# Kernel tuning notes

Hardware: AMD Instinct MI355X
Metric: run time of the kernel (lower is better)

The kernel has to match this reference:

```python
import jax, jax.numpy as jnp
import numpy as np

RADII = (4, 8, 16)
BETA = 0.3
TEMP = 0.07
EPS = 1e-6


def box_filter(x, r):
    """Windowed sum over a (2r+1)x(2r+1) window with zero padding (same as
    F.conv2d with a ones kernel and padding=r), applied to the last two axes.
    Uses cumulative sums (integral image) instead of an explicit convolution."""
    def along(x, axis):
        n = x.shape[axis]
        c = jnp.cumsum(x, axis=axis)
        pad = [(0, 0)] * x.ndim
        pad[axis] = (1, 0)
        c = jnp.pad(c, pad)  # prepend a zero so c[i] = sum of first i elems
        i = jnp.arange(n)
        hi = jnp.clip(i + r + 1, 0, n)
        lo = jnp.clip(i - r, 0, n)
        return jnp.take(c, hi, axis=axis) - jnp.take(c, lo, axis=axis)
    return along(along(x, -2), -1)


def build_prototypes(support_feats, mask_f, anchor_pos, anchor_sample, anchor_radius):
    """mask_f: [S,H,W] float. Returns (local_protos [M,C], local_weights [M], global_proto [C])."""
    fg = mask_f.sum()
    global_proto = (support_feats * mask_f[:, None]).sum((0, 2, 3)) / (fg + EPS)

    masked = support_feats * mask_f[:, None]  # [S,C,H,W]
    means, msums = [], []
    for r in RADII:
        fsum = box_filter(masked, r)              # [S,C,H,W] windowed masked feature sum
        msum = box_filter(mask_f, r)              # [S,H,W]   windowed fg pixel count
        means.append(fsum / (msum[:, None] + EPS))
        msums.append(msum)
    mean = jnp.stack(means)   # [R,S,C,H,W] windowed masked means per radius
    msum = jnp.stack(msums)   # [R,S,H,W]

    y, x = anchor_pos[:, 0], anchor_pos[:, 1]
    local_protos = mean[anchor_radius, anchor_sample, :, y, x]   # [M,C]
    local_weights = msum[anchor_radius, anchor_sample, y, x]     # [M]
    local_weights = local_weights / (local_weights.sum() + EPS)
    return local_protos, local_weights, global_proto


def _l2norm(x, axis):
    n = jnp.sqrt(jnp.sum(x * x, axis=axis, keepdims=True))
    return x / jnp.maximum(n, 1e-12)


def reference(support_feats, support_masks, query_feats, anchor_pos, anchor_sample, anchor_radius):
    mask_f = support_masks.astype(support_feats.dtype)[:, 0]  # [S,H,W]
    protos, weights, gproto = build_prototypes(
        support_feats, mask_f, anchor_pos, anchor_sample, anchor_radius)

    q_norm = _l2norm(query_feats, axis=1)                     # [B,C,H,W]
    g = _l2norm(gproto[None], axis=1)[0]                      # [C]
    s_global = jnp.einsum('bchw,c->bhw', q_norm, g)

    p_norm = _l2norm(protos, axis=1)                          # [M,C]
    sims = jnp.einsum('bchw,mc->bmhw', q_norm, p_norm)        # [B,M,H,W]
    w = weights / (weights.sum() + EPS)
    local_score = jnp.einsum('bmhw,m->bhw', sims, w)

    s_fg = BETA * s_global + (1.0 - BETA) * local_score
    logits = jnp.stack((-s_fg / TEMP, s_fg / TEMP), axis=1)   # [B,2,H,W]
    return logits


def setup_inputs() -> dict:
    key = jax.random.key(0)
    k1, k2, k3, k4, k5, k6 = jax.random.split(key, 6)
    S, C, H, W = 4, 384, 96, 96
    B, M = 8, 64
    return {
        'support_feats': jax.random.normal(k1, (S, C, H, W), dtype=jnp.float32),
        'support_masks': jax.random.randint(k2, (S, 1, H, W), 0, 2, dtype=jnp.int32),
        'query_feats': jax.random.normal(k3, (B, C, H, W), dtype=jnp.float32),
        'anchor_pos': jax.random.randint(k4, (M, 2), 0, H, dtype=jnp.int32),
        'anchor_sample': jax.random.randint(k5, (M,), 0, S, dtype=jnp.int32),
        'anchor_radius': jax.random.randint(k6, (M,), 0, len(RADII), dtype=jnp.int32),
    }
```

## Files before the change

kernel.cpp:

```cpp
#include <hip/hip_runtime.h>
#include <math.h>

#define S_ 4
#define C_ 384
#define H_ 96
#define W_ 96
#define B_ 8
#define M_ 64
#define HW_ (H_ * W_)
#define EPSV 1e-6f
#define BETA_V 0.3f
#define TEMP_V 0.07f

#define NB_PLANE (S_ * C_)
#define NB_PREP (NB_PLANE + M_ + 1)

#define NCH 32
#define CCH (C_ / NCH)
#define NPART 3
#define PT (HW_ / NPART)
#define NB_S1 (B_ * NCH * NPART)
#define NB_S2 (B_ * HW_ / 256)

__device__ __forceinline__ float wave_sum(float v) {
#pragma unroll
    for (int o = 32; o; o >>= 1) v += __shfl_down(v, o, 64);
    return v;
}

__device__ __forceinline__ float block_sum(float v) {
    __shared__ float sm[4];
    int lane = threadIdx.x & 63;
    int wid = threadIdx.x >> 6;
    v = wave_sum(v);
    if (lane == 0) sm[wid] = v;
    __syncthreads();
    float r = sm[0] + sm[1] + sm[2] + sm[3];
    __syncthreads();
    return r;
}

__global__ __launch_bounds__(256) void k_prep(const float* __restrict__ feats,
                                              const int* __restrict__ mask,
                                              const int* __restrict__ pos,
                                              const int* __restrict__ samp,
                                              const int* __restrict__ rad,
                                              float* __restrict__ partial,
                                              float* __restrict__ praw,
                                              float* __restrict__ msum_out,
                                              float* __restrict__ fg_out) {
    int bid = blockIdx.x;
    int t = threadIdx.x;

    if (bid < NB_PLANE) {
        __shared__ float mplane[HW_];
        int s = bid / C_;
        int c = bid - s * C_;
        const float4* fp = (const float4*)(feats + (size_t)bid * HW_);
        const int4* mp = (const int4*)(mask + (size_t)s * HW_);
        float acc = 0.0f;
#pragma unroll
        for (int k = 0; k < HW_ / 4 / 256; ++k) {
            int i = t + k * 256;
            float4 f = fp[i];
            int4 m = mp[i];
            float4 w;
            w.x = f.x * (float)m.x;
            w.y = f.y * (float)m.y;
            w.z = f.z * (float)m.z;
            w.w = f.w * (float)m.w;
            acc += w.x + w.y + w.z + w.w;
            ((float4*)mplane)[i] = w;
        }
        float tot = block_sum(acc);
        if (t == 0) partial[bid] = tot;

        int wid = t >> 6;
        int lane = t & 63;
        for (int a = wid; a < M_; a += 4) {
            if (samp[a] != s) continue;
            int y = pos[2 * a + 0];
            int x = pos[2 * a + 1];
            int ri = rad[a];
            int r = (ri == 0) ? 4 : (ri == 1) ? 8 : 16;
            int y0 = max(y - r, 0), y1 = min(y + r + 1, H_);
            int x0 = max(x - r, 0), x1 = min(x + r + 1, W_);
            int ww = x1 - x0;
            int n = (y1 - y0) * ww;
            float a2 = 0.0f;
            int yy = lane / ww;
            int xx = lane - yy * ww;
            int dy = 64 / ww, dx = 64 - dy * ww;
            for (int i = lane; i < n; i += 64) {
                a2 += mplane[(y0 + yy) * W_ + x0 + xx];
                xx += dx; yy += dy;
                if (xx >= ww) { xx -= ww; ++yy; }
            }
            a2 = wave_sum(a2);
            if (lane == 0) praw[a * C_ + c] = a2;
        }
        return;
    }
    bid -= NB_PLANE;
    if (bid < M_) {
        int a = bid;
        int y = pos[2 * a + 0];
        int x = pos[2 * a + 1];
        int s = samp[a];
        int ri = rad[a];
        int r = (ri == 0) ? 4 : (ri == 1) ? 8 : 16;
        int y0 = max(y - r, 0), y1 = min(y + r + 1, H_);
        int x0 = max(x - r, 0), x1 = min(x + r + 1, W_);
        int ww = x1 - x0;
        int n = (y1 - y0) * ww;
        const int* mp = mask + (size_t)s * HW_;
        float macc = 0.0f;
        int yy = t / ww;
        int xx = t - yy * ww;
        int dy = 256 / ww, dx = 256 - dy * ww;
        for (int i = t; i < n; i += 256) {
            macc += (float)mp[(y0 + yy) * W_ + x0 + xx];
            xx += dx; yy += dy;
            if (xx >= ww) { xx -= ww; ++yy; }
        }
        float ms = block_sum(macc);
        if (t == 0) msum_out[a] = ms;
        return;
    }
    const int4* mp4 = (const int4*)mask;
    float acc = 0.0f;
    for (int i = t; i < S_ * HW_ / 4; i += 256) {
        int4 m = mp4[i];
        acc += (float)(m.x + m.y + m.z + m.w);
    }
    float fg = block_sum(acc);
    if (t == 0) fg_out[0] = fg;
}

__global__ __launch_bounds__(256) void k_finalize(const float* __restrict__ partial,
                                                  const float* __restrict__ msum,
                                                  const float* __restrict__ praw,
                                                  const float* __restrict__ fg_in,
                                                  float* __restrict__ v) {
    int tid = threadIdx.x;
    int wid = tid >> 6;
    int lane = tid & 63;

    float invfg = 1.0f / (fg_in[0] + EPSV);

    __shared__ float gv[C_];
    for (int c = tid; c < C_; c += 256) {
        float tv = 0.0f;
        for (int s = 0; s < S_; ++s) tv += partial[s * C_ + c];
        gv[c] = tv * invfg;
    }
    __syncthreads();

    float sq = 0.0f;
    for (int c = tid; c < C_; c += 256) sq += gv[c] * gv[c];
    float gn = block_sum(sq);
    gn = fmaxf(sqrtf(gn), 1e-12f);

    float wa = (tid < M_) ? msum[tid] : 0.0f;
    float T = block_sum(wa);
    float wb = (tid < M_) ? msum[tid] / (T + EPSV) : 0.0f;
    float wsum = block_sum(wb);

    __shared__ float pn[M_];
    for (int m = wid; m < M_; m += 4) {
        float im = 1.0f / (msum[m] + EPSV);
        float a = 0.0f;
        for (int c = lane; c < C_; c += 64) {
            float p = praw[m * C_ + c] * im;
            a += p * p;
        }
        a = wave_sum(a);
        if (lane == 0) pn[m] = fmaxf(sqrtf(a), 1e-12f);
    }
    __syncthreads();

    __shared__ float wq[M_];
    if (tid < M_) {
        float w = (msum[tid] / (T + EPSV)) / (wsum + EPSV);
        wq[tid] = w / pn[tid] * (1.0f / (msum[tid] + EPSV));
    }
    __syncthreads();

    for (int c = tid; c < C_; c += 256) {
        float vl = 0.0f;
        for (int m = 0; m < M_; ++m) vl += wq[m] * praw[m * C_ + c];
        v[c] = BETA_V * (gv[c] / gn) + (1.0f - BETA_V) * vl;
    }
}

__global__ __launch_bounds__(256) void k_score1(const float* __restrict__ q,
                                                const float* __restrict__ v,
                                                float* __restrict__ wsd,
                                                float* __restrict__ wss) {
    int bid = blockIdx.x;
    int part = bid % NPART;
    int bc = bid / NPART;
    int ch = bc % NCH;
    int b = bc / NCH;
    int t = threadIdx.x;
    int pxb = part * PT;

    float vcs[CCH];
#pragma unroll
    for (int j = 0; j < CCH; ++j) vcs[j] = v[ch * CCH + j];

    float4 d0 = {0.f, 0.f, 0.f, 0.f}, d1 = d0, d2 = d0;
    float4 s0 = d0, s1 = d0, s2 = d0;
#pragma unroll 2
    for (int j = 0; j < CCH; ++j) {
        int c = ch * CCH + j;
        float vc = vcs[j];
        const float4* qc = (const float4*)(q + ((size_t)b * C_ + c) * HW_ + pxb);
        float4 f0 = qc[0 * 256 + t];
        float4 f1 = qc[1 * 256 + t];
        float4 f2 = qc[2 * 256 + t];
        d0.x += f0.x * vc; d0.y += f0.y * vc; d0.z += f0.z * vc; d0.w += f0.w * vc;
        s0.x += f0.x * f0.x; s0.y += f0.y * f0.y; s0.z += f0.z * f0.z; s0.w += f0.w * f0.w;
        d1.x += f1.x * vc; d1.y += f1.y * vc; d1.z += f1.z * vc; d1.w += f1.w * vc;
        s1.x += f1.x * f1.x; s1.y += f1.y * f1.y; s1.z += f1.z * f1.z; s1.w += f1.w * f1.w;
        d2.x += f2.x * vc; d2.y += f2.y * vc; d2.z += f2.z * vc; d2.w += f2.w * vc;
        s2.x += f2.x * f2.x; s2.y += f2.y * f2.y; s2.z += f2.z * f2.z; s2.w += f2.w * f2.w;
    }

    size_t base = ((size_t)(b * NCH + ch) * HW_ + pxb) / 4;
    float4* od = (float4*)wsd;
    float4* os = (float4*)wss;
    od[base + 0 * 256 + t] = d0;
    od[base + 1 * 256 + t] = d1;
    od[base + 2 * 256 + t] = d2;
    os[base + 0 * 256 + t] = s0;
    os[base + 1 * 256 + t] = s1;
    os[base + 2 * 256 + t] = s2;
}

__global__ __launch_bounds__(256) void k_score2(const float* __restrict__ wsd,
                                                const float* __restrict__ wss,
                                                float* __restrict__ out) {
    int px = blockIdx.x * 256 + threadIdx.x;
    int b = px / HW_;
    int p = px - b * HW_;

    float d = 0.0f, s2 = 0.0f;
#pragma unroll
    for (int ch = 0; ch < NCH; ++ch) {
        size_t idx = (size_t)(b * NCH + ch) * HW_ + p;
        d += wsd[idx];
        s2 += wss[idx];
    }
    float sv = d / fmaxf(sqrtf(s2), 1e-12f);
    float o = sv / TEMP_V;
    float* ob = out + (size_t)b * 2 * HW_;
    ob[p] = -o;
    ob[HW_ + p] = o;
}

extern "C" void kernel_launch(void* const* d_in, const int* in_sizes, int n_in,
                              void* d_out, int out_size, void* d_ws, size_t ws_size,
                              hipStream_t stream) {
    const float* support_feats = (const float*)d_in[0];
    const int* support_masks = (const int*)d_in[1];
    const float* query_feats = (const float*)d_in[2];
    const int* anchor_pos = (const int*)d_in[3];
    const int* anchor_sample = (const int*)d_in[4];
    const int* anchor_radius = (const int*)d_in[5];
    float* out = (float*)d_out;

    float* ws = (float*)d_ws;
    float* ws_partial = ws;
    float* ws_msum = ws_partial + S_ * C_;
    float* ws_praw = ws_msum + M_;
    float* ws_v = ws_praw + M_ * C_;
    float* ws_fg = ws_v + C_;
    float* ws_dot = ws_fg + 1;
    float* ws_sq = ws_dot + (size_t)B_ * NCH * HW_;

    k_prep<<<NB_PREP, 256, 0, stream>>>(support_feats, support_masks, anchor_pos,
                                        anchor_sample, anchor_radius,
                                        ws_partial, ws_praw, ws_msum, ws_fg);
    k_finalize<<<1, 256, 0, stream>>>(ws_partial, ws_msum, ws_praw, ws_fg, ws_v);
    k_score1<<<NB_S1, 256, 0, stream>>>(query_feats, ws_v, ws_dot, ws_sq);
    k_score2<<<NB_S2, 256, 0, stream>>>(ws_dot, ws_sq, out);
}
```

Measured before the change: 98.87 us.

## Split per-anchor prototype sums into dedicated blocks instead of per-plane scans

Per-anchor window sums were previously computed inside each (sample, channel) plane block, which staged the full masked plane in 36KB of shared memory and looped over every anchor. The anchor sums now run in separate blocks, one per (anchor, group of 4 channels). Each of these blocks loads the window mask into a small shared buffer and reads the feature window directly. This removes the large shared-memory footprint and the serial anchor loop from the global-sum blocks, raising occupancy there. The cost is more blocks, and the feature windows are read again from global memory. The normalization by the mask count moves into the prep kernel.

```diff
diff --git a/kernel.cpp b/kernel.cpp
--- a/kernel.cpp
+++ b/kernel.cpp
@@ -12,8 +12,9 @@
 #define BETA_V 0.3f
 #define TEMP_V 0.07f
 
-#define NB_PLANE (S_ * C_)
-#define NB_PREP (NB_PLANE + M_ + 1)
+#define NB_A (S_ * C_)
+#define NB_B (M_ * (C_ / 4))
+#define NB_PREP (NB_A + NB_B + 1)
 
 #define NCH 32
 #define CCH (C_ / NCH)
@@ -46,16 +47,14 @@
                                               const int* __restrict__ samp,
                                               const int* __restrict__ rad,
                                               float* __restrict__ partial,
-                                              float* __restrict__ praw,
+                                              float* __restrict__ proto,
                                               float* __restrict__ msum_out,
                                               float* __restrict__ fg_out) {
     int bid = blockIdx.x;
     int t = threadIdx.x;
 
-    if (bid < NB_PLANE) {
-        __shared__ float mplane[HW_];
+    if (bid < NB_A) {
         int s = bid / C_;
-        int c = bid - s * C_;
         const float4* fp = (const float4*)(feats + (size_t)bid * HW_);
         const int4* mp = (const int4*)(mask + (size_t)s * HW_);
         float acc = 0.0f;
@@ -64,67 +63,63 @@
             int i = t + k * 256;
             float4 f = fp[i];
             int4 m = mp[i];
-            float4 w;
-            w.x = f.x * (float)m.x;
-            w.y = f.y * (float)m.y;
-            w.z = f.z * (float)m.z;
-            w.w = f.w * (float)m.w;
-            acc += w.x + w.y + w.z + w.w;
-            ((float4*)mplane)[i] = w;
+            acc += f.x * (float)m.x + f.y * (float)m.y + f.z * (float)m.z + f.w * (float)m.w;
         }
         float tot = block_sum(acc);
         if (t == 0) partial[bid] = tot;
-
-        int wid = t >> 6;
-        int lane = t & 63;
-        for (int a = wid; a < M_; a += 4) {
-            if (samp[a] != s) continue;
-            int y = pos[2 * a + 0];
-            int x = pos[2 * a + 1];
-            int ri = rad[a];
-            int r = (ri == 0) ? 4 : (ri == 1) ? 8 : 16;
-            int y0 = max(y - r, 0), y1 = min(y + r + 1, H_);
-            int x0 = max(x - r, 0), x1 = min(x + r + 1, W_);
-            int ww = x1 - x0;
-            int n = (y1 - y0) * ww;
-            float a2 = 0.0f;
-            int yy = lane / ww;
-            int xx = lane - yy * ww;
-            int dy = 64 / ww, dx = 64 - dy * ww;
-            for (int i = lane; i < n; i += 64) {
-                a2 += mplane[(y0 + yy) * W_ + x0 + xx];
-                xx += dx; yy += dy;
-                if (xx >= ww) { xx -= ww; ++yy; }
-            }
-            a2 = wave_sum(a2);
-            if (lane == 0) praw[a * C_ + c] = a2;
-        }
         return;
     }
-    bid -= NB_PLANE;
-    if (bid < M_) {
-        int a = bid;
-        int y = pos[2 * a + 0];
-        int x = pos[2 * a + 1];
-        int s = samp[a];
-        int ri = rad[a];
+    bid -= NB_A;
+    if (bid < NB_B) {
+        const int CG = C_ / 4;
+        int m = bid / CG;
+        int cg = bid % CG;
+        int y = pos[2 * m + 0];
+        int x = pos[2 * m + 1];
+        int s = samp[m];
+        int ri = rad[m];
         int r = (ri == 0) ? 4 : (ri == 1) ? 8 : 16;
         int y0 = max(y - r, 0), y1 = min(y + r + 1, H_);
         int x0 = max(x - r, 0), x1 = min(x + r + 1, W_);
         int ww = x1 - x0;
         int n = (y1 - y0) * ww;
+
+        __shared__ float mwin[33 * 33];
         const int* mp = mask + (size_t)s * HW_;
         float macc = 0.0f;
-        int yy = t / ww;
-        int xx = t - yy * ww;
-        int dy = 256 / ww, dx = 256 - dy * ww;
-        for (int i = t; i < n; i += 256) {
-            macc += (float)mp[(y0 + yy) * W_ + x0 + xx];
-            xx += dx; yy += dy;
-            if (xx >= ww) { xx -= ww; ++yy; }
-        }
-        float ms = block_sum(macc);
-        if (t == 0) msum_out[a] = ms;
+        {
+            int yy = t / ww;
+            int xx = t - yy * ww;
+            int dy = 256 / ww, dx = 256 - dy * ww;
+            for (int i = t; i < n; i += 256) {
+                float mv = (float)mp[(y0 + yy) * W_ + x0 + xx];
+                mwin[i] = mv;
+                macc += mv;
+                xx += dx; yy += dy;
+                if (xx >= ww) { xx -= ww; ++yy; }
+            }
+        }
+        float msumv = block_sum(macc);
+        if (cg == 0 && t == 0) msum_out[m] = msumv;
+        float inv = 1.0f / (msumv + EPSV);
+
+        int wid = t >> 6;
+        int lane = t & 63;
+        int c = cg * 4 + wid;
+        const float* fp = feats + ((size_t)s * C_ + c) * HW_;
+        float acc = 0.0f;
+        {
+            int yy = lane / ww;
+            int xx = lane - yy * ww;
+            int dy = 64 / ww, dx = 64 - dy * ww;
+            for (int i = lane; i < n; i += 64) {
+                acc += fp[(y0 + yy) * W_ + x0 + xx] * mwin[i];
+                xx += dx; yy += dy;
+                if (xx >= ww) { xx -= ww; ++yy; }
+            }
+        }
+        acc = wave_sum(acc);
+        if (lane == 0) proto[m * C_ + c] = acc * inv;
         return;
     }
     const int4* mp4 = (const int4*)mask;
@@ -139,7 +134,7 @@
 
 __global__ __launch_bounds__(256) void k_finalize(const float* __restrict__ partial,
                                                   const float* __restrict__ msum,
-                                                  const float* __restrict__ praw,
+                                                  const float* __restrict__ proto,
                                                   const float* __restrict__ fg_in,
                                                   float* __restrict__ v) {
     int tid = threadIdx.x;
@@ -168,10 +163,9 @@
 
     __shared__ float pn[M_];
     for (int m = wid; m < M_; m += 4) {
-        float im = 1.0f / (msum[m] + EPSV);
         float a = 0.0f;
         for (int c = lane; c < C_; c += 64) {
-            float p = praw[m * C_ + c] * im;
+            float p = proto[m * C_ + c];
             a += p * p;
         }
         a = wave_sum(a);
@@ -182,13 +176,13 @@
     __shared__ float wq[M_];
     if (tid < M_) {
         float w = (msum[tid] / (T + EPSV)) / (wsum + EPSV);
-        wq[tid] = w / pn[tid] * (1.0f / (msum[tid] + EPSV));
+        wq[tid] = w / pn[tid];
     }
     __syncthreads();
 
     for (int c = tid; c < C_; c += 256) {
         float vl = 0.0f;
-        for (int m = 0; m < M_; ++m) vl += wq[m] * praw[m * C_ + c];
+        for (int m = 0; m < M_; ++m) vl += wq[m] * proto[m * C_ + c];
         v[c] = BETA_V * (gv[c] / gn) + (1.0f - BETA_V) * vl;
     }
 }
@@ -273,16 +267,16 @@
     float* ws = (float*)d_ws;
     float* ws_partial = ws;
     float* ws_msum = ws_partial + S_ * C_;
-    float* ws_praw = ws_msum + M_;
-    float* ws_v = ws_praw + M_ * C_;
+    float* ws_proto = ws_msum + M_;
+    float* ws_v = ws_proto + M_ * C_;
     float* ws_fg = ws_v + C_;
     float* ws_dot = ws_fg + 1;
     float* ws_sq = ws_dot + (size_t)B_ * NCH * HW_;
 
     k_prep<<<NB_PREP, 256, 0, stream>>>(support_feats, support_masks, anchor_pos,
                                         anchor_sample, anchor_radius,
-                                        ws_partial, ws_praw, ws_msum, ws_fg);
-    k_finalize<<<1, 256, 0, stream>>>(ws_partial, ws_msum, ws_praw, ws_fg, ws_v);
+                                        ws_partial, ws_proto, ws_msum, ws_fg);
+    k_finalize<<<1, 256, 0, stream>>>(ws_partial, ws_msum, ws_proto, ws_fg, ws_v);
     k_score1<<<NB_S1, 256, 0, stream>>>(query_feats, ws_v, ws_dot, ws_sq);
     k_score2<<<NB_S2, 256, 0, stream>>>(ws_dot, ws_sq, out);
 }
```

After: 101.5 us. +2.6%, slower.
